# Optimization experiments

Measured on AMD Instinct MI355X. Metric: run time of the kernel, lower is better.

Reference implementation:

```python
import jax, jax.numpy as jnp
import numpy as np

B, S, H = 2, 2048, 1024
NH, NKV, HD = 16, 4, 64
G, R = NKV, NH // NKV  # 4 kv groups, 4 query heads per group


def setup_inputs() -> dict:
    key = jax.random.key(0)
    ks = jax.random.split(key, 7)
    scale = 1.0 / np.sqrt(H)
    return {
        "hidden_states": jax.random.normal(ks[0], (B, S, H), jnp.float32),
        "cos": jax.random.normal(ks[1], (S, HD), jnp.float32),
        "sin": jax.random.normal(ks[2], (S, HD), jnp.float32),
        "attention_mask": jnp.ones((B, S), jnp.float32),
        "Wq": jax.random.normal(ks[3], (H, NH * HD), jnp.float32) * scale,
        "Wk": jax.random.normal(ks[4], (H, NKV * HD), jnp.float32) * scale,
        "Wv": jax.random.normal(ks[5], (H, NKV * HD), jnp.float32) * scale,
        "Wo": jax.random.normal(ks[6], (NH * HD, H), jnp.float32) * scale,
    }


def _rotate_half(x):
    h = x.shape[-1] // 2
    return jnp.concatenate([-x[..., h:], x[..., :h]], axis=-1)


def reference(hidden_states, cos, sin, attention_mask, Wq, Wk, Wv, Wo):
    x = hidden_states
    q = (x @ Wq).reshape(B, S, NH, HD)
    k = (x @ Wk).reshape(B, S, NKV, HD)
    v = (x @ Wv).reshape(B, S, NKV, HD)
    # RoPE: cos/sin [S,HD] broadcast over batch and heads
    c = cos[None, :, None, :]
    s = sin[None, :, None, :]
    q = q * c + _rotate_half(q) * s
    k = k * c + _rotate_half(k) * s
    # GQA without materializing repeated KV: q grouped as [B,S,G,R,HD]
    qg = q.reshape(B, S, G, R, HD)
    scores = jnp.einsum("bsgrd,btgd->bgrst", qg, k) / np.sqrt(HD)  # [B,G,R,S,T]
    causal = jnp.tril(jnp.ones((S, S), bool))
    scores = jnp.where(causal[None, None, None], scores, -jnp.inf)
    scores = scores + ((1.0 - attention_mask) * -1e9)[:, None, None, None, :]
    probs = jax.nn.softmax(scores.astype(jnp.float32), axis=-1).astype(q.dtype)
    out = jnp.einsum("bgrst,btgd->bsgrd", probs, v).reshape(B, S, NH * HD)
    return out @ Wo
```

## Files before the change

kernel.cpp:

```cpp
#include <hip/hip_runtime.h>
#include <math.h>

#define B_   2
#define S_   2048
#define H_   1024
#define NH_  16
#define NKV_ 4
#define HD_  64
#define R_   (NH_ / NKV_)
#define QKVW 1536

typedef __attribute__((ext_vector_type(8))) short bf16x8;
typedef __attribute__((ext_vector_type(4))) float f32x4;

__device__ inline short f2bf(float f) {
    unsigned u = __float_as_uint(f);
    u += 0x7FFF + ((u >> 16) & 1);
    return (short)(u >> 16);
}

__device__ inline void gload_lds16(const void* gptr, void* lptr) {
    __builtin_amdgcn_global_load_lds(
        (const __attribute__((address_space(1))) unsigned int*)gptr,
        (__attribute__((address_space(3))) unsigned int*)lptr,
        16, 0, 0);
}

__global__ __launch_bounds__(256) void tconv_all(const float* __restrict__ Wq,
                                                 const float* __restrict__ Wk,
                                                 const float* __restrict__ Wv,
                                                 const float* __restrict__ Wo,
                                                 short* __restrict__ Wqkvt,
                                                 short* __restrict__ Wot) {
    __shared__ short T[64][68];
    const int bx = blockIdx.x;
    const float* W; short* Wt; int N, idx;
    if (bx < 256)      { W = Wq; Wt = Wqkvt;                     N = 1024; idx = bx; }
    else if (bx < 320) { W = Wk; Wt = Wqkvt + 1024 * 1024;       N = 256;  idx = bx - 256; }
    else if (bx < 384) { W = Wv; Wt = Wqkvt + 1280 * 1024;       N = 256;  idx = bx - 320; }
    else               { W = Wo; Wt = Wot;                       N = 1024; idx = bx - 384; }
    const int ntiles = N >> 6;
    const int n0 = (idx % ntiles) * 64;
    const int k0 = (idx / ntiles) * 64;

    const int tid = threadIdx.x;
    const int r  = tid >> 4;
    const int c4 = (tid & 15) * 4;
#pragma unroll
    for (int t = 0; t < 4; t++) {
        int row = t * 16 + r;
        float4 v = *(const float4*)&W[(size_t)(k0 + row) * N + n0 + c4];
        T[c4 + 0][row] = f2bf(v.x);
        T[c4 + 1][row] = f2bf(v.y);
        T[c4 + 2][row] = f2bf(v.z);
        T[c4 + 3][row] = f2bf(v.w);
    }
    __syncthreads();
#pragma unroll
    for (int t = 0; t < 4; t++) {
        int row = t * 16 + r;
        short4 o = *(short4*)&T[row][c4];
        *(short4*)&Wt[(size_t)(n0 + row) * 1024 + k0 + c4] = o;
    }
}

__global__ __launch_bounds__(256) void gemm1_fused(const float* __restrict__ x,
                                                   const short* __restrict__ Bt,
                                                   short* __restrict__ qkv,
                                                   short* __restrict__ Vtg,
                                                   const float* __restrict__ cosb,
                                                   const float* __restrict__ sinb) {
    __shared__ short Ah[64 * 32];
    __shared__ short Bh[128 * 32];

    const int tid  = threadIdx.x;
    const int w    = tid >> 6;
    const int lane = tid & 63;
    const int ln   = lane & 15;
    const int qd   = lane >> 4;
    const int wr   = w >> 1, wc = w & 1;
    const int row0 = blockIdx.y * 64;
    const int col0 = blockIdx.x * 128;

    const int sr = lane >> 2;
    const int sk = (lane & 3) * 8;
    const int ar  = tid >> 2;
    const int ac8 = (tid & 3) * 8;

    f32x4 acc[2][4];
#pragma unroll
    for (int mi = 0; mi < 2; mi++)
#pragma unroll
        for (int ni = 0; ni < 4; ni++)
            acc[mi][ni] = (f32x4){0.f, 0.f, 0.f, 0.f};

    for (int k0 = 0; k0 < 1024; k0 += 32) {
        __syncthreads();
        {
            const float* xp = x + (size_t)(row0 + ar) * H_ + k0 + ac8;
            float4 a = *(const float4*)xp;
            float4 b2 = *(const float4*)(xp + 4);
            bf16x8 o;
            o[0] = f2bf(a.x);  o[1] = f2bf(a.y);  o[2] = f2bf(a.z);  o[3] = f2bf(a.w);
            o[4] = f2bf(b2.x); o[5] = f2bf(b2.y); o[6] = f2bf(b2.z); o[7] = f2bf(b2.w);
            *(bf16x8*)&Ah[ar * 32 + ac8] = o;
        }
        gload_lds16(Bt + (size_t)(col0 + w * 32 + sr) * 1024 + k0 + sk, &Bh[(w * 32) * 32]);
        gload_lds16(Bt + (size_t)(col0 + w * 32 + 16 + sr) * 1024 + k0 + sk, &Bh[(w * 32 + 16) * 32]);
        __syncthreads();

        bf16x8 af[2], bfr[4];
#pragma unroll
        for (int mi = 0; mi < 2; mi++)
            af[mi] = *(const bf16x8*)&Ah[(wr * 32 + mi * 16 + ln) * 32 + qd * 8];
#pragma unroll
        for (int ni = 0; ni < 4; ni++)
            bfr[ni] = *(const bf16x8*)&Bh[(wc * 64 + ni * 16 + ln) * 32 + qd * 8];
#pragma unroll
        for (int mi = 0; mi < 2; mi++)
#pragma unroll
            for (int ni = 0; ni < 4; ni++)
                acc[mi][ni] = __builtin_amdgcn_mfma_f32_16x16x32_bf16(af[mi], bfr[ni], acc[mi][ni], 0, 0, 0);
    }

    const int colw = col0 + wc * 64;
    if (colw < H_ + NKV_ * HD_) {
#pragma unroll
        for (int mi = 0; mi < 2; mi++)
#pragma unroll
            for (int i = 0; i < 4; i++) {
                const int row  = row0 + wr * 32 + mi * 16 + qd * 4 + i;
                const int spos = row & (S_ - 1);
                const float* cp = cosb + (size_t)spos * HD_;
                const float* sp = sinb + (size_t)spos * HD_;
                float o0[4];
#pragma unroll
                for (int ni = 0; ni < 2; ni++) {
                    const int d = ni * 16 + ln;
                    float x0 = acc[mi][ni][i], x1 = acc[mi][ni + 2][i];
                    o0[ni]     = x0 * cp[d]      - x1 * sp[d];
                    o0[ni + 2] = x1 * cp[d + 32] + x0 * sp[d + 32];
                }
                short* Cp = qkv + (size_t)row * QKVW + colw + ln;
#pragma unroll
                for (int ni = 0; ni < 4; ni++) Cp[ni * 16] = f2bf(o0[ni]);
            }
    } else {
        const int g = (colw - (H_ + NKV_ * HD_)) >> 6;
#pragma unroll
        for (int mi = 0; mi < 2; mi++) {
            const int rbase = row0 + wr * 32 + mi * 16 + qd * 4;
            const int bg = ((rbase >> 11) * NKV_) + g;
            const int s0 = rbase & (S_ - 1);
#pragma unroll
            for (int ni = 0; ni < 4; ni++) {
                const int d = ni * 16 + ln;
                short4 pk = { f2bf(acc[mi][ni][0]), f2bf(acc[mi][ni][1]),
                              f2bf(acc[mi][ni][2]), f2bf(acc[mi][ni][3]) };
                *(short4*)&Vtg[((size_t)bg * HD_ + d) * S_ + s0] = pk;
            }
        }
    }
}

__global__ __launch_bounds__(256) void gemm2_bt(const short* __restrict__ A, int lda,
                                                const short* __restrict__ Bt,
                                                float* __restrict__ C, int ldc,
                                                int K) {
    __shared__ short Ah[64 * 32];
    __shared__ short Bh[128 * 32];

    const int tid  = threadIdx.x;
    const int w    = tid >> 6;
    const int lane = tid & 63;
    const int ln   = lane & 15;
    const int qd   = lane >> 4;
    const int wr   = w >> 1, wc = w & 1;
    const int row0 = blockIdx.y * 64;
    const int col0 = blockIdx.x * 128;

    const int sr = lane >> 2;
    const int sk = (lane & 3) * 8;

    f32x4 acc[2][4];
#pragma unroll
    for (int mi = 0; mi < 2; mi++)
#pragma unroll
        for (int ni = 0; ni < 4; ni++)
            acc[mi][ni] = (f32x4){0.f, 0.f, 0.f, 0.f};

    for (int k0 = 0; k0 < K; k0 += 32) {
        __syncthreads();
        gload_lds16(A + (size_t)(row0 + w * 16 + sr) * lda + k0 + sk, &Ah[(w * 16) * 32]);
        gload_lds16(Bt + (size_t)(col0 + w * 32 + sr) * K + k0 + sk, &Bh[(w * 32) * 32]);
        gload_lds16(Bt + (size_t)(col0 + w * 32 + 16 + sr) * K + k0 + sk, &Bh[(w * 32 + 16) * 32]);
        __syncthreads();

        bf16x8 af[2], bfr[4];
#pragma unroll
        for (int mi = 0; mi < 2; mi++)
            af[mi] = *(const bf16x8*)&Ah[(wr * 32 + mi * 16 + ln) * 32 + qd * 8];
#pragma unroll
        for (int ni = 0; ni < 4; ni++)
            bfr[ni] = *(const bf16x8*)&Bh[(wc * 64 + ni * 16 + ln) * 32 + qd * 8];
#pragma unroll
        for (int mi = 0; mi < 2; mi++)
#pragma unroll
            for (int ni = 0; ni < 4; ni++)
                acc[mi][ni] = __builtin_amdgcn_mfma_f32_16x16x32_bf16(af[mi], bfr[ni], acc[mi][ni], 0, 0, 0);
    }

#pragma unroll
    for (int mi = 0; mi < 2; mi++)
#pragma unroll
        for (int i = 0; i < 4; i++) {
            const size_t row = row0 + wr * 32 + mi * 16 + qd * 4 + i;
            float* Cp = C + row * ldc + col0 + wc * 64 + ln;
#pragma unroll
            for (int ni = 0; ni < 4; ni++) Cp[ni * 16] = acc[mi][ni][i];
        }
}

__global__ __launch_bounds__(256) void attn_kernel(short* __restrict__ qkv,
                                                   const short* __restrict__ Vtg,
                                                   const float* __restrict__ maskb) {
    const int tid  = threadIdx.x;
    const int w    = tid >> 6;
    const int lane = tid & 63;
    const int ln   = lane & 15;
    const int qd   = lane >> 4;

    const int by = blockIdx.y;
    const int b  = by / NH_;
    const int h  = by % NH_;
    const int g  = h / R_;
    const int bg = b * NKV_ + g;
    const int qt = (by & 1) ? (15 - (int)blockIdx.x) : (int)blockIdx.x;
    const int q0 = qt * 128;
    const int rowb = q0 + w * 32;

    __shared__ short Ks[2][64 * 72];
    __shared__ short Vt[2][64 * 72];
    __shared__ short Ps[4 * 32 * 72];
    __shared__ float mskS[2][64];

    const int f0r = tid >> 3,         f0c = (tid & 7) * 8;
    const int f1r = (tid + 256) >> 3, f1c = ((tid + 256) & 7) * 8;

    bf16x8 qf[2][2];
#pragma unroll
    for (int rg = 0; rg < 2; rg++) {
        const short* qp = qkv + (size_t)(b * S_ + rowb + rg * 16 + ln) * QKVW + h * HD_;
        qf[rg][0] = *(const bf16x8*)&qp[qd * 8];
        qf[rg][1] = *(const bf16x8*)&qp[32 + qd * 8];
    }

    f32x4 O[2][4] = {};
    float mrow[2] = {-1e30f, -1e30f};
    float lrow[2] = {0.0f, 0.0f};

    const int ktiles = 2 * qt + 2;

    {
        *(bf16x8*)&Ks[0][f0r * 72 + f0c] =
            *(const bf16x8*)&qkv[(size_t)(b * S_ + f0r) * QKVW + H_ + g * HD_ + f0c];
        *(bf16x8*)&Ks[0][f1r * 72 + f1c] =
            *(const bf16x8*)&qkv[(size_t)(b * S_ + f1r) * QKVW + H_ + g * HD_ + f1c];
        *(bf16x8*)&Vt[0][f0r * 72 + f0c] =
            *(const bf16x8*)&Vtg[((size_t)bg * HD_ + f0r) * S_ + f0c];
        *(bf16x8*)&Vt[0][f1r * 72 + f1c] =
            *(const bf16x8*)&Vtg[((size_t)bg * HD_ + f1r) * S_ + f1c];
        if (tid < 64) mskS[0][tid] = maskb[b * S_ + tid];
    }
    __syncthreads();

    int cur = 0;
    for (int kt = 0; kt < ktiles; kt++) {
        const int base = kt * 64;
        const bool pf = (kt + 1 < ktiles);

        bf16x8 pk0, pk1, pv0, pv1;
        float pm = 0.0f;
        if (pf) {
            const int nb = base + 64;
            pk0 = *(const bf16x8*)&qkv[(size_t)(b * S_ + nb + f0r) * QKVW + H_ + g * HD_ + f0c];
            pk1 = *(const bf16x8*)&qkv[(size_t)(b * S_ + nb + f1r) * QKVW + H_ + g * HD_ + f1c];
            pv0 = *(const bf16x8*)&Vtg[((size_t)bg * HD_ + f0r) * S_ + nb + f0c];
            pv1 = *(const bf16x8*)&Vtg[((size_t)bg * HD_ + f1r) * S_ + nb + f1c];
            if (tid < 64) pm = maskb[b * S_ + nb + tid];
        }

        if (base <= rowb + 31) {
            f32x4 St[2][4];
#pragma unroll
            for (int kg = 0; kg < 4; kg++) {
                bf16x8 ka0 = *(const bf16x8*)&Ks[cur][(kg * 16 + ln) * 72 + qd * 8];
                bf16x8 ka1 = *(const bf16x8*)&Ks[cur][(kg * 16 + ln) * 72 + 32 + qd * 8];
#pragma unroll
                for (int rg = 0; rg < 2; rg++) {
                    f32x4 z = {0.f, 0.f, 0.f, 0.f};
                    z = __builtin_amdgcn_mfma_f32_16x16x32_bf16(ka0, qf[rg][0], z, 0, 0, 0);
                    St[rg][kg] = __builtin_amdgcn_mfma_f32_16x16x32_bf16(ka1, qf[rg][1], z, 0, 0, 0);
                }
            }

            float mt[4][4];
#pragma unroll
            for (int kg = 0; kg < 4; kg++) {
                float4 mv = *(const float4*)&mskS[cur][kg * 16 + qd * 4];
                mt[kg][0] = (1.0f - mv.x) * -1e9f;
                mt[kg][1] = (1.0f - mv.y) * -1e9f;
                mt[kg][2] = (1.0f - mv.z) * -1e9f;
                mt[kg][3] = (1.0f - mv.w) * -1e9f;
            }

#pragma unroll
            for (int rg = 0; rg < 2; rg++) {
                const int qrow = rowb + rg * 16 + ln;
                float sc[4][4];
#pragma unroll
                for (int kg = 0; kg < 4; kg++) {
                    const int keyb = base + kg * 16 + qd * 4;
#pragma unroll
                    for (int i = 0; i < 4; i++) {
                        float v = St[rg][kg][i] * 0.125f + mt[kg][i];
                        sc[kg][i] = (keyb + i <= qrow) ? v : -1e30f;
                    }
                }
                float mx = sc[0][0];
#pragma unroll
                for (int kg = 0; kg < 4; kg++)
#pragma unroll
                    for (int i = 0; i < 4; i++) mx = fmaxf(mx, sc[kg][i]);
                mx = fmaxf(mx, __shfl_xor(mx, 16));
                mx = fmaxf(mx, __shfl_xor(mx, 32));

                float nm = fmaxf(mrow[rg], mx);
                if (__ballot(nm > mrow[rg])) {
                    float alpha = __expf(mrow[rg] - nm);
                    lrow[rg] *= alpha;
#pragma unroll
                    for (int i = 0; i < 4; i++) {
                        float av = __shfl(alpha, qd * 4 + i);
#pragma unroll
                        for (int dt = 0; dt < 4; dt++) O[rg][dt][i] *= av;
                    }
                }
                mrow[rg] = nm;

                float ls = 0.0f;
                float pr[4][4];
#pragma unroll
                for (int kg = 0; kg < 4; kg++)
#pragma unroll
                    for (int i = 0; i < 4; i++) {
                        float p = __expf(sc[kg][i] - nm);
                        pr[kg][i] = p;
                        ls += p;
                    }
                ls += __shfl_xor(ls, 16);
                ls += __shfl_xor(ls, 32);
                lrow[rg] += ls;

#pragma unroll
                for (int kg = 0; kg < 4; kg++) {
                    short4 pk = { f2bf(pr[kg][0]), f2bf(pr[kg][1]),
                                  f2bf(pr[kg][2]), f2bf(pr[kg][3]) };
                    *(short4*)&Ps[w * 2304 + (rg * 16 + ln) * 72 + kg * 16 + qd * 4] = pk;
                }
            }

#pragma unroll
            for (int kc2 = 0; kc2 < 2; kc2++) {
                bf16x8 pa0 = *(const bf16x8*)&Ps[w * 2304 + (ln)      * 72 + kc2 * 32 + qd * 8];
                bf16x8 pa1 = *(const bf16x8*)&Ps[w * 2304 + (16 + ln) * 72 + kc2 * 32 + qd * 8];
#pragma unroll
                for (int dt = 0; dt < 4; dt++) {
                    bf16x8 vb = *(const bf16x8*)&Vt[cur][(dt * 16 + ln) * 72 + kc2 * 32 + qd * 8];
                    O[0][dt] = __builtin_amdgcn_mfma_f32_16x16x32_bf16(pa0, vb, O[0][dt], 0, 0, 0);
                    O[1][dt] = __builtin_amdgcn_mfma_f32_16x16x32_bf16(pa1, vb, O[1][dt], 0, 0, 0);
                }
            }
        }

        if (pf) {
            const int nxt = cur ^ 1;
            *(bf16x8*)&Ks[nxt][f0r * 72 + f0c] = pk0;
            *(bf16x8*)&Ks[nxt][f1r * 72 + f1c] = pk1;
            *(bf16x8*)&Vt[nxt][f0r * 72 + f0c] = pv0;
            *(bf16x8*)&Vt[nxt][f1r * 72 + f1c] = pv1;
            if (tid < 64) mskS[nxt][tid] = pm;
        }
        __syncthreads();
        cur ^= 1;
    }

#pragma unroll
    for (int rg = 0; rg < 2; rg++)
#pragma unroll
        for (int i = 0; i < 4; i++) {
            float li  = __shfl(lrow[rg], qd * 4 + i);
            float inv = 1.0f / li;
            const int row = rowb + rg * 16 + qd * 4 + i;
            short* op = qkv + (size_t)(b * S_ + row) * QKVW + h * HD_ + ln;
#pragma unroll
            for (int dt = 0; dt < 4; dt++) op[dt * 16] = f2bf(O[rg][dt][i] * inv);
        }
}

extern "C" void kernel_launch(void* const* d_in, const int* in_sizes, int n_in,
                              void* d_out, int out_size, void* d_ws, size_t ws_size,
                              hipStream_t stream) {
    const float* x     = (const float*)d_in[0];
    const float* cosb  = (const float*)d_in[1];
    const float* sinb  = (const float*)d_in[2];
    const float* maskb = (const float*)d_in[3];
    const float* Wq    = (const float*)d_in[4];
    const float* Wk    = (const float*)d_in[5];
    const float* Wv    = (const float*)d_in[6];
    const float* Wo    = (const float*)d_in[7];

    const int M = B_ * S_;

    short* qkv   = (short*)d_ws;
    short* Wqkvt = qkv + (size_t)M * QKVW;
    short* Wot   = Wqkvt + (size_t)QKVW * H_;
    short* Vtg   = Wot + (size_t)H_ * H_;
    float* out   = (float*)d_out;

    dim3 blk(256);

    tconv_all<<<dim3(640), blk, 0, stream>>>(Wq, Wk, Wv, Wo, Wqkvt, Wot);

    gemm1_fused<<<dim3(QKVW / 128, M / 64), blk, 0, stream>>>(x, Wqkvt, qkv, Vtg, cosb, sinb);

    attn_kernel<<<dim3(S_ / 128, B_ * NH_), blk, 0, stream>>>(qkv, Vtg, maskb);

    gemm2_bt<<<dim3(H_ / 128, M / 64), blk, 0, stream>>>(qkv, QKVW, Wot, out, H_, H_);
}
```

Measured before the change: 227.2 us.

## Restructure attention into per-warp independent tiles reading K/V directly from global

Rewrites the attention kernel so each block handles paired query tiles (a and 15-a) for balanced causal work, launched as 256 blocks. K, V and mask are loaded straight from global into registers per warp rather than staged through double-buffered LDS with block-wide barriers. Each warp iterates only the key tiles it needs and applies the causal mask only on the diagonal tile. The online-softmax rescale is skipped unless the running max grows by more than 8, which trades exactness of the max for fewer rescales. It also relies on L2/L1 for K/V reuse across warps instead of shared memory.

```diff
diff --git a/kernel.cpp b/kernel.cpp
--- a/kernel.cpp
+++ b/kernel.cpp
@@ -230,90 +230,78 @@
     const int ln   = lane & 15;
     const int qd   = lane >> 4;
 
-    const int by = blockIdx.y;
-    const int b  = by / NH_;
-    const int h  = by % NH_;
-    const int g  = h / R_;
-    const int bg = b * NKV_ + g;
-    const int qt = (by & 1) ? (15 - (int)blockIdx.x) : (int)blockIdx.x;
-    const int q0 = qt * 128;
-    const int rowb = q0 + w * 32;
-
-    __shared__ short Ks[2][64 * 72];
-    __shared__ short Vt[2][64 * 72];
-    __shared__ short Ps[4 * 32 * 72];
-    __shared__ float mskS[2][64];
-
-    const int f0r = tid >> 3,         f0c = (tid & 7) * 8;
-    const int f1r = (tid + 256) >> 3, f1c = ((tid + 256) & 7) * 8;
-
-    bf16x8 qf[2][2];
-#pragma unroll
-    for (int rg = 0; rg < 2; rg++) {
-        const short* qp = qkv + (size_t)(b * S_ + rowb + rg * 16 + ln) * QKVW + h * HD_;
-        qf[rg][0] = *(const bf16x8*)&qp[qd * 8];
-        qf[rg][1] = *(const bf16x8*)&qp[32 + qd * 8];
-    }
-
-    f32x4 O[2][4] = {};
-    float mrow[2] = {-1e30f, -1e30f};
-    float lrow[2] = {0.0f, 0.0f};
-
-    const int ktiles = 2 * qt + 2;
-
-    {
-        *(bf16x8*)&Ks[0][f0r * 72 + f0c] =
-            *(const bf16x8*)&qkv[(size_t)(b * S_ + f0r) * QKVW + H_ + g * HD_ + f0c];
-        *(bf16x8*)&Ks[0][f1r * 72 + f1c] =
-            *(const bf16x8*)&qkv[(size_t)(b * S_ + f1r) * QKVW + H_ + g * HD_ + f1c];
-        *(bf16x8*)&Vt[0][f0r * 72 + f0c] =
-            *(const bf16x8*)&Vtg[((size_t)bg * HD_ + f0r) * S_ + f0c];
-        *(bf16x8*)&Vt[0][f1r * 72 + f1c] =
-            *(const bf16x8*)&Vtg[((size_t)bg * HD_ + f1r) * S_ + f1c];
-        if (tid < 64) mskS[0][tid] = maskb[b * S_ + tid];
-    }
-    __syncthreads();
-
-    int cur = 0;
-    for (int kt = 0; kt < ktiles; kt++) {
-        const int base = kt * 64;
-        const bool pf = (kt + 1 < ktiles);
-
-        bf16x8 pk0, pk1, pv0, pv1;
-        float pm = 0.0f;
-        if (pf) {
-            const int nb = base + 64;
-            pk0 = *(const bf16x8*)&qkv[(size_t)(b * S_ + nb + f0r) * QKVW + H_ + g * HD_ + f0c];
-            pk1 = *(const bf16x8*)&qkv[(size_t)(b * S_ + nb + f1r) * QKVW + H_ + g * HD_ + f1c];
-            pv0 = *(const bf16x8*)&Vtg[((size_t)bg * HD_ + f0r) * S_ + nb + f0c];
-            pv1 = *(const bf16x8*)&Vtg[((size_t)bg * HD_ + f1r) * S_ + nb + f1c];
-            if (tid < 64) pm = maskb[b * S_ + nb + tid];
+    const int fid = blockIdx.x;
+    const int bg  = fid & 7;
+    const int u   = fid >> 3;
+    const int b   = bg >> 2;
+    const int g   = bg & 3;
+    const int h   = g * R_ + (u & 3);
+    const int a   = u >> 2;
+
+    __shared__ short Ps[4][32 * 72];
+    short* const ps = Ps[w];
+
+    const short* const Kb = qkv + H_ + g * HD_;
+
+    for (int half = 0; half < 2; half++) {
+        const int qt   = half ? (15 - a) : a;
+        const int ws   = half ? (3 - w) : w;
+        const int rowb = qt * 128 + ws * 32;
+        const int nt   = (rowb >> 6) + 1;
+
+        bf16x8 qf[2][2];
+#pragma unroll
+        for (int rg = 0; rg < 2; rg++) {
+            const short* qp = qkv + (size_t)(b * S_ + rowb + rg * 16 + ln) * QKVW + h * HD_;
+            qf[rg][0] = *(const bf16x8*)&qp[qd * 8];
+            qf[rg][1] = *(const bf16x8*)&qp[32 + qd * 8];
         }
 
-        if (base <= rowb + 31) {
-            f32x4 St[2][4];
+        f32x4 O[2][4] = {};
+        float mrow[2] = {-1e30f, -1e30f};
+        float lrow[2] = {0.0f, 0.0f};
+
+        for (int kt = 0; kt < nt; kt++) {
+            const int base = kt * 64;
+
+            bf16x8 ka0[4], ka1[4];
 #pragma unroll
             for (int kg = 0; kg < 4; kg++) {
-                bf16x8 ka0 = *(const bf16x8*)&Ks[cur][(kg * 16 + ln) * 72 + qd * 8];
-                bf16x8 ka1 = *(const bf16x8*)&Ks[cur][(kg * 16 + ln) * 72 + 32 + qd * 8];
-#pragma unroll
-                for (int rg = 0; rg < 2; rg++) {
-                    f32x4 z = {0.f, 0.f, 0.f, 0.f};
-                    z = __builtin_amdgcn_mfma_f32_16x16x32_bf16(ka0, qf[rg][0], z, 0, 0, 0);
-                    St[rg][kg] = __builtin_amdgcn_mfma_f32_16x16x32_bf16(ka1, qf[rg][1], z, 0, 0, 0);
-                }
-            }
+                const short* kp = Kb + (size_t)(b * S_ + base + kg * 16 + ln) * QKVW;
+                ka0[kg] = *(const bf16x8*)&kp[qd * 8];
+                ka1[kg] = *(const bf16x8*)&kp[32 + qd * 8];
+            }
+            bf16x8 vb[2][4];
+#pragma unroll
+            for (int kc2 = 0; kc2 < 2; kc2++)
+#pragma unroll
+                for (int dt = 0; dt < 4; dt++)
+                    vb[kc2][dt] = *(const bf16x8*)
+                        &Vtg[((size_t)bg * HD_ + dt * 16 + ln) * S_ + base + kc2 * 32 + qd * 8];
 
             float mt[4][4];
 #pragma unroll
             for (int kg = 0; kg < 4; kg++) {
-                float4 mv = *(const float4*)&mskS[cur][kg * 16 + qd * 4];
+                float4 mv = *(const float4*)&maskb[b * S_ + base + kg * 16 + qd * 4];
                 mt[kg][0] = (1.0f - mv.x) * -1e9f;
                 mt[kg][1] = (1.0f - mv.y) * -1e9f;
                 mt[kg][2] = (1.0f - mv.z) * -1e9f;
                 mt[kg][3] = (1.0f - mv.w) * -1e9f;
             }
 
+            f32x4 St[2][4];
+#pragma unroll
+            for (int kg = 0; kg < 4; kg++) {
+#pragma unroll
+                for (int rg = 0; rg < 2; rg++) {
+                    f32x4 z = {0.f, 0.f, 0.f, 0.f};
+                    z = __builtin_amdgcn_mfma_f32_16x16x32_bf16(ka0[kg], qf[rg][0], z, 0, 0, 0);
+                    St[rg][kg] = __builtin_amdgcn_mfma_f32_16x16x32_bf16(ka1[kg], qf[rg][1], z, 0, 0, 0);
+                }
+            }
+
+            const bool diag = (kt == nt - 1);
+
 #pragma unroll
             for (int rg = 0; rg < 2; rg++) {
                 const int qrow = rowb + rg * 16 + ln;
@@ -323,8 +311,8 @@
                     const int keyb = base + kg * 16 + qd * 4;
 #pragma unroll
                     for (int i = 0; i < 4; i++) {
-                        float v = St[rg][kg][i] * 0.125f + mt[kg][i];
-                        sc[kg][i] = (keyb + i <= qrow) ? v : -1e30f;
+                        float v = fmaf(St[rg][kg][i], 0.125f, mt[kg][i]);
+                        sc[kg][i] = (diag && (keyb + i > qrow)) ? -1e30f : v;
                     }
                 }
                 float mx = sc[0][0];
@@ -335,8 +323,8 @@
                 mx = fmaxf(mx, __shfl_xor(mx, 16));
                 mx = fmaxf(mx, __shfl_xor(mx, 32));
 
-                float nm = fmaxf(mrow[rg], mx);
-                if (__ballot(nm > mrow[rg])) {
+                if (__ballot(mx > mrow[rg] + 8.0f)) {
+                    float nm    = fmaxf(mrow[rg], mx);
                     float alpha = __expf(mrow[rg] - nm);
                     lrow[rg] *= alpha;
 #pragma unroll
@@ -345,8 +333,9 @@
 #pragma unroll
                         for (int dt = 0; dt < 4; dt++) O[rg][dt][i] *= av;
                     }
-                }
-                mrow[rg] = nm;
+                    mrow[rg] = nm;
+                }
+                const float nm = mrow[rg];
 
                 float ls = 0.0f;
                 float pr[4][4];
@@ -366,46 +355,34 @@
                 for (int kg = 0; kg < 4; kg++) {
                     short4 pk = { f2bf(pr[kg][0]), f2bf(pr[kg][1]),
                                   f2bf(pr[kg][2]), f2bf(pr[kg][3]) };
-                    *(short4*)&Ps[w * 2304 + (rg * 16 + ln) * 72 + kg * 16 + qd * 4] = pk;
+                    *(short4*)&ps[(rg * 16 + ln) * 72 + kg * 16 + qd * 4] = pk;
                 }
             }
 
 #pragma unroll
             for (int kc2 = 0; kc2 < 2; kc2++) {
-                bf16x8 pa0 = *(const bf16x8*)&Ps[w * 2304 + (ln)      * 72 + kc2 * 32 + qd * 8];
-                bf16x8 pa1 = *(const bf16x8*)&Ps[w * 2304 + (16 + ln) * 72 + kc2 * 32 + qd * 8];
+                bf16x8 pa0 = *(const bf16x8*)&ps[(ln)      * 72 + kc2 * 32 + qd * 8];
+                bf16x8 pa1 = *(const bf16x8*)&ps[(16 + ln) * 72 + kc2 * 32 + qd * 8];
 #pragma unroll
                 for (int dt = 0; dt < 4; dt++) {
-                    bf16x8 vb = *(const bf16x8*)&Vt[cur][(dt * 16 + ln) * 72 + kc2 * 32 + qd * 8];
-                    O[0][dt] = __builtin_amdgcn_mfma_f32_16x16x32_bf16(pa0, vb, O[0][dt], 0, 0, 0);
-                    O[1][dt] = __builtin_amdgcn_mfma_f32_16x16x32_bf16(pa1, vb, O[1][dt], 0, 0, 0);
+                    O[0][dt] = __builtin_amdgcn_mfma_f32_16x16x32_bf16(pa0, vb[kc2][dt], O[0][dt], 0, 0, 0);
+                    O[1][dt] = __builtin_amdgcn_mfma_f32_16x16x32_bf16(pa1, vb[kc2][dt], O[1][dt], 0, 0, 0);
                 }
             }
         }
 
-        if (pf) {
-            const int nxt = cur ^ 1;
-            *(bf16x8*)&Ks[nxt][f0r * 72 + f0c] = pk0;
-            *(bf16x8*)&Ks[nxt][f1r * 72 + f1c] = pk1;
-            *(bf16x8*)&Vt[nxt][f0r * 72 + f0c] = pv0;
-            *(bf16x8*)&Vt[nxt][f1r * 72 + f1c] = pv1;
-            if (tid < 64) mskS[nxt][tid] = pm;
-        }
-        __syncthreads();
-        cur ^= 1;
-    }
-
-#pragma unroll
-    for (int rg = 0; rg < 2; rg++)
-#pragma unroll
-        for (int i = 0; i < 4; i++) {
-            float li  = __shfl(lrow[rg], qd * 4 + i);
-            float inv = 1.0f / li;
-            const int row = rowb + rg * 16 + qd * 4 + i;
-            short* op = qkv + (size_t)(b * S_ + row) * QKVW + h * HD_ + ln;
-#pragma unroll
-            for (int dt = 0; dt < 4; dt++) op[dt * 16] = f2bf(O[rg][dt][i] * inv);
-        }
+#pragma unroll
+        for (int rg = 0; rg < 2; rg++)
+#pragma unroll
+            for (int i = 0; i < 4; i++) {
+                float li  = __shfl(lrow[rg], qd * 4 + i);
+                float inv = 1.0f / li;
+                const int row = rowb + rg * 16 + qd * 4 + i;
+                short* op = qkv + (size_t)(b * S_ + row) * QKVW + h * HD_ + ln;
+#pragma unroll
+                for (int dt = 0; dt < 4; dt++) op[dt * 16] = f2bf(O[rg][dt][i] * inv);
+            }
+    }
 }
 
 extern "C" void kernel_launch(void* const* d_in, const int* in_sizes, int n_in,
@@ -434,7 +411,7 @@
 
     gemm1_fused<<<dim3(QKVW / 128, M / 64), blk, 0, stream>>>(x, Wqkvt, qkv, Vtg, cosb, sinb);
 
-    attn_kernel<<<dim3(S_ / 128, B_ * NH_), blk, 0, stream>>>(qkv, Vtg, maskb);
+    attn_kernel<<<dim3(256), blk, 0, stream>>>(qkv, Vtg, maskb);
 
     gemm2_bt<<<dim3(H_ / 128, M / 64), blk, 0, stream>>>(qkv, QKVW, Wot, out, H_, H_);
 }
```

Measured after the change: 204.3 us. 1.11x faster.
